# Optimization experiments

Measured on AMD Instinct MI355X. Metric: run time of the kernel, lower is better.

## Reference

```python
import jax, jax.numpy as jnp
import numpy as np

EPS = 1e-5
NUM_HEADS = 8
GN_GROUPS = 32


def _hardswish(x):
    return x * jnp.clip(x + 3.0, 0.0, 6.0) / 6.0


def setup_inputs() -> dict:
    key = jax.random.key(0)
    ks = jax.random.split(key, 12)
    B, C, H, W = 2, 256, 56, 56
    mid, inner = 32, 64  # mid_ca=max(C//8,32); inner=max(C//8, 8*8)//8*8
    s = 0.02
    return {
        "x": jax.random.normal(ks[0], (B, C, H, W), jnp.float32),
        "gate_conv_w": jax.random.normal(ks[1], (mid, C), jnp.float32) * s,
        "bn_gamma": jnp.ones((mid,), jnp.float32),
        "bn_beta": jnp.zeros((mid,), jnp.float32),
        "bn_mean": jax.random.normal(ks[2], (mid,), jnp.float32) * 0.1,
        "bn_var": jax.random.uniform(ks[3], (mid,), jnp.float32) + 0.5,
        "gate_h_w": jax.random.normal(ks[4], (C, mid), jnp.float32) * s,
        "gate_w_w": jax.random.normal(ks[5], (C, mid), jnp.float32) * s,
        "proj_in_w": jax.random.normal(ks[6], (inner, C), jnp.float32) * s,
        "ln_gamma": jnp.ones((inner,), jnp.float32),
        "ln_beta": jnp.zeros((inner,), jnp.float32),
        "wq": jax.random.normal(ks[7], (inner, inner), jnp.float32) * s,
        "wk": jax.random.normal(ks[8], (inner, inner), jnp.float32) * s,
        "wv": jax.random.normal(ks[9], (inner, inner), jnp.float32) * s,
        "proj_out_w": jax.random.normal(ks[10], (C, inner), jnp.float32) * s,
        "gn_gamma": jnp.ones((C,), jnp.float32),
        "gn_beta": jnp.zeros((C,), jnp.float32),
    }


def reference(x, gate_conv_w, bn_gamma, bn_beta, bn_mean, bn_var,
              gate_h_w, gate_w_w, proj_in_w, ln_gamma, ln_beta,
              wq, wk, wv, proj_out_w, gn_gamma, gn_beta):
    B, C, H, W = x.shape
    N = H * W
    inner = proj_in_w.shape[0]
    dh = inner // NUM_HEADS
    scale = dh ** (-0.5)

    # ---- CA gate: pool along W and H, shared 1x1 conv + BN(eval) + hardswish ----
    h_pool = x.mean(axis=3)                      # (B,C,H)
    w_pool = x.mean(axis=2)                      # (B,C,W)
    cat = jnp.concatenate([h_pool, w_pool], axis=2)          # (B,C,H+W)
    cat = jnp.einsum('mc,bcl->bml', gate_conv_w, cat)        # 1x1 conv
    cat = (cat - bn_mean[:, None]) * jax.lax.rsqrt(bn_var[:, None] + EPS)
    cat = cat * bn_gamma[:, None] + bn_beta[:, None]
    cat = _hardswish(cat)
    g_h, g_w = cat[:, :, :H], cat[:, :, H:]                  # (B,mid,H), (B,mid,W)
    gate_h = jax.nn.sigmoid(jnp.einsum('cm,bmh->bch', gate_h_w, g_h))  # (B,C,H)
    gate_w = jax.nn.sigmoid(jnp.einsum('cm,bmw->bcw', gate_w_w, g_w))  # (B,C,W)
    gate = gate_h[:, :, :, None] * gate_w[:, :, None, :]     # (B,C,H,W)

    # ---- projection + layernorm over channel dim ----
    seq = jnp.einsum('ic,bchw->bhwi', proj_in_w, x).reshape(B, N, inner)
    mu = seq.mean(-1, keepdims=True)
    var = seq.var(-1, keepdims=True)  # biased, as torch LayerNorm
    seq = (seq - mu) * jax.lax.rsqrt(var + EPS) * ln_gamma + ln_beta

    gate_spatial = gate.mean(axis=1).reshape(B, N)           # (B,N)

    def heads(w):
        return (seq @ w.T).reshape(B, N, NUM_HEADS, dh).transpose(0, 2, 1, 3)
    q, k, v = heads(wq), heads(wk), heads(wv)                # (B,h,N,dh)

    scores = jnp.einsum('bhnd,bhmd->bhnm', q, k) * scale     # (B,h,N,N)
    gate_bias = jnp.maximum(jnp.log(gate_spatial), -5.0)[:, None, None, :]
    attn = jax.nn.softmax(scores + gate_bias, axis=-1)
    out = jnp.einsum('bhnm,bhmd->bhnd', attn, v)             # (B,h,N,dh)
    out = out.transpose(0, 2, 1, 3).reshape(B, N, inner)
    out = out.transpose(0, 2, 1).reshape(B, inner, H, W)
    out = jnp.einsum('ci,bihw->bchw', proj_out_w, out)       # proj_out 1x1 conv

    # ---- GroupNorm(32, C) ----
    og = out.reshape(B, GN_GROUPS, C // GN_GROUPS, H, W)
    gmu = og.mean((2, 3, 4), keepdims=True)
    gvar = og.var((2, 3, 4), keepdims=True)
    og = (og - gmu) * jax.lax.rsqrt(gvar + EPS)
    out = og.reshape(B, C, H, W) * gn_gamma[None, :, None, None] + gn_beta[None, :, None, None]

    return x + out
```

## Files before the change

kernel.cpp:

```cpp
#include <hip/hip_runtime.h>
#include <math.h>

#define EPSF 1e-5f

constexpr int B_ = 2, C_ = 256, H_ = 56, W_ = 56, N_ = 3136;
constexpr int MID_ = 32, L_ = 112, IN_ = 64, NH_ = 8;

typedef __attribute__((ext_vector_type(8))) __bf16 bf16x8;
typedef __attribute__((ext_vector_type(16))) float f32x16;

constexpr size_t O_POOL = 0;
constexpr size_t O_GH   = O_POOL + (size_t)B_*C_*L_;
constexpr size_t O_GW   = O_GH   + (size_t)B_*C_*H_;
constexpr size_t O_QT   = O_GW   + (size_t)B_*C_*W_;
constexpr size_t O_KT   = O_QT   + (size_t)B_*NH_*N_*16/2;
constexpr size_t O_VT   = O_KT   + (size_t)B_*NH_*N_*16/2;
constexpr size_t O_VZ   = O_VT   + (size_t)B_*NH_*16*N_/2;
constexpr size_t O_OUTC = O_VZ   + N_/2;
constexpr size_t O_GST  = O_OUTC + (size_t)B_*C_*N_/2;
constexpr size_t O_PART = O_GST  + (size_t)B_*32*2;

__device__ inline unsigned pkbf(float lo, float hi) {
  __bf16 a = (__bf16)lo, c = (__bf16)hi;
  return (unsigned)__builtin_bit_cast(unsigned short, a)
       | ((unsigned)__builtin_bit_cast(unsigned short, c) << 16);
}

__device__ inline float bf2f(unsigned short u) {
  unsigned v = (unsigned)u << 16;
  return __builtin_bit_cast(float, v);
}

__device__ inline float fast_exp2(float x) {
#if __has_builtin(__builtin_amdgcn_exp2f)
  return __builtin_amdgcn_exp2f(x);
#else
  float r; asm("v_exp_f32 %0, %1" : "=v"(r) : "v"(x)); return r;
#endif
}

__device__ inline void plane32_swap(unsigned &a, unsigned &b) {
#if __has_builtin(__builtin_amdgcn_permlane32_swap)
  typedef unsigned uv2 __attribute__((ext_vector_type(2)));
  uv2 r = __builtin_amdgcn_permlane32_swap(a, b, false, false);
  a = r.x; b = r.y;
#else
  asm volatile("v_permlane32_swap_b32 %0, %1" : "+v"(a), "+v"(b));
#endif
}

__global__ __launch_bounds__(256) void k_pool(const float* __restrict__ x, float* __restrict__ pool) {
  int bc = blockIdx.x;
  const float4* xp4 = reinterpret_cast<const float4*>(x + (size_t)bc * N_);
  __shared__ float tile[N_];
  float4* t4 = reinterpret_cast<float4*>(tile);
  for (int i = threadIdx.x; i < N_/4; i += 256) t4[i] = xp4[i];
  __syncthreads();
  int t = threadIdx.x;
  if (t < 224) {
    int o = t >> 1, half = t & 1;
    float r = 0.f;
    if (o < 56) {
      const float* row = tile + o*W_ + half*28;
      #pragma unroll 7
      for (int j = 0; j < 28; ++j) r += row[j];
    } else {
      const float* col = tile + (half*28)*W_ + (o - 56);
      #pragma unroll 7
      for (int j = 0; j < 28; ++j) r += col[j*W_];
    }
    r += __shfl_xor(r, 1);
    if (half == 0) pool[(size_t)bc*L_ + o] = r * (1.f/56.f);
  }
}

__global__ __launch_bounds__(256) void k_gates2(const float* __restrict__ gcw, const float* __restrict__ pool,
    const float* __restrict__ bng, const float* __restrict__ bnb,
    const float* __restrict__ bnm, const float* __restrict__ bnv,
    const float* __restrict__ ghw, const float* __restrict__ gww,
    float* __restrict__ ghT, float* __restrict__ gwT) {
  int b = blockIdx.x / H_;
  int p = blockIdx.x % H_;
  __shared__ float cat_s[2][MID_];
  int t = threadIdx.x;
  {
    int out = t >> 2, sub = t & 3;
    int m = out & 31, which = out >> 5;
    int l = p + which*H_;
    const float* pp = pool + (size_t)b*C_*L_ + l;
    const float* wp = gcw + (size_t)m*C_ + sub*64;
    float s = 0.f;
    #pragma unroll 16
    for (int c = 0; c < 64; ++c) s += wp[c] * pp[(size_t)(sub*64 + c)*L_];
    s += __shfl_xor(s, 1); s += __shfl_xor(s, 2);
    if (sub == 0) {
      float xn = (s - bnm[m]) * rsqrtf(bnv[m] + EPSF) * bng[m] + bnb[m];
      cat_s[which][m] = xn * fminf(fmaxf(xn + 3.f, 0.f), 6.f) * (1.f/6.f);
    }
  }
  __syncthreads();
  int c = t;
  float sh = 0.f, sw = 0.f;
  #pragma unroll 8
  for (int m = 0; m < MID_; ++m) {
    sh += ghw[c*MID_ + m] * cat_s[0][m];
    sw += gww[c*MID_ + m] * cat_s[1][m];
  }
  ghT[((size_t)b*H_ + p)*C_ + c] = 1.f/(1.f + expf(-sh));
  gwT[((size_t)b*W_ + p)*C_ + c] = 1.f/(1.f + expf(-sw));
}

__global__ __launch_bounds__(256) void k_fused(const float* __restrict__ x,
    const float* __restrict__ piw, const float* __restrict__ lng, const float* __restrict__ lnb,
    const float* __restrict__ wq, const float* __restrict__ wk, const float* __restrict__ wv,
    const float* __restrict__ ghT, const float* __restrict__ gwT,
    unsigned short* __restrict__ qt, unsigned short* __restrict__ kt,
    unsigned short* __restrict__ vt, unsigned short* __restrict__ vz,
    float* __restrict__ gst) {
  __shared__ __align__(16) unsigned short sT[64][72];
  __shared__ float ps[2][2][64][2];
  __shared__ float lg[64], lb[64];
  __shared__ float bias_s[64];
  int b = blockIdx.x / 49, n0 = (blockIdx.x % 49) * 64;
  int tid = threadIdx.x;
  int wv_ = tid >> 6, lane = tid & 63;
  int m = wv_ & 1, nh = wv_ >> 1, l31 = lane & 31, g = lane >> 5;
  int nloc = nh*32 + l31;
  int nglob = n0 + nloc;
  const float QS = 0.35355339059327373f * 1.4426950408889634f;

  if (tid < 64) { lg[tid] = lng[tid]; lb[tid] = lnb[tid]; }
  if (blockIdx.x == 0 && tid < B_*32*2) gst[tid] = 0.f;

  {
    int px = tid >> 2, sub = tid & 3;
    int n = n0 + px;
    int h = n / W_, w = n % W_;
    const float4* gh4 = reinterpret_cast<const float4*>(ghT + ((size_t)b*H_ + h)*C_ + sub*64);
    const float4* gw4 = reinterpret_cast<const float4*>(gwT + ((size_t)b*W_ + w)*C_ + sub*64);
    float s = 0.f;
    #pragma unroll
    for (int i = 0; i < 16; ++i) {
      float4 a = gh4[i], c2 = gw4[i];
      s += a.x*c2.x + a.y*c2.y + a.z*c2.z + a.w*c2.w;
    }
    s += __shfl_xor(s, 1); s += __shfl_xor(s, 2);
    if (sub == 0)
      bias_s[px] = fmaxf(logf(s * (1.f/C_)), -5.f) * 1.4426950408889634f;
  }
  __syncthreads();

  for (int u = tid; u < 512; u += 256) {
    int h = u >> 6, n = u & 63;
    size_t base = ((size_t)(b*NH_ + h)*N_ + n0 + n)*16;
    *reinterpret_cast<uint4*>(qt + base + 8) = make_uint4(0x3F803F80u, 0u, 0u, 0u);
    float bv = bias_s[n];
    __bf16 bhi = (__bf16)bv; float blo = bv - (float)bhi;
    *reinterpret_cast<uint4*>(kt + base + 8) = make_uint4(pkbf((float)bhi, blo), 0u, 0u, 0u);
  }
  for (int u = tid; u < 512; u += 256) {
    int rr = u >> 3, chunk = u & 7;
    int h = rr >> 3, r = 8 + (rr & 7);
    unsigned val = (r == 8 || r == 12) ? 0x3F803F80u : 0u;
    *reinterpret_cast<uint4*>(vt + ((size_t)(b*NH_+h)*16 + r)*N_ + n0 + chunk*8)
        = make_uint4(val, val, val, val);
  }
  if (b == 0 && tid < 8)
    *reinterpret_cast<uint4*>(vz + n0 + tid*8) = make_uint4(0u, 0u, 0u, 0u);

  const float* arow = piw + (size_t)(32*m + l31)*C_;
  const float* xcol = x + (size_t)b*C_*N_ + nglob;
  f32x16 acc;
  #pragma unroll
  for (int i = 0; i < 16; ++i) acc[i] = 0.f;
  #pragma unroll 4
  for (int kk = 0; kk < 16; ++kk) {
    const float4* ap = reinterpret_cast<const float4*>(arow + kk*16 + g*8);
    float4 a0 = ap[0], a1 = ap[1];
    uint4 au;
    au.x = pkbf(a0.x, a0.y); au.y = pkbf(a0.z, a0.w);
    au.z = pkbf(a1.x, a1.y); au.w = pkbf(a1.z, a1.w);
    float bvl[8];
    #pragma unroll
    for (int e = 0; e < 8; ++e) bvl[e] = xcol[(size_t)(kk*16 + g*8 + e)*N_];
    uint4 bu;
    bu.x = pkbf(bvl[0], bvl[1]); bu.y = pkbf(bvl[2], bvl[3]);
    bu.z = pkbf(bvl[4], bvl[5]); bu.w = pkbf(bvl[6], bvl[7]);
    acc = __builtin_amdgcn_mfma_f32_32x32x16_bf16(
        __builtin_bit_cast(bf16x8, au), __builtin_bit_cast(bf16x8, bu), acc, 0, 0, 0);
  }

  float s = 0.f, ss = 0.f;
  #pragma unroll
  for (int i = 0; i < 16; ++i) { s += acc[i]; ss += acc[i]*acc[i]; }
  ps[m][g][nloc][0] = s; ps[m][g][nloc][1] = ss;
  __syncthreads();
  float S  = ps[0][0][nloc][0] + ps[0][1][nloc][0] + ps[1][0][nloc][0] + ps[1][1][nloc][0];
  float SS = ps[0][0][nloc][1] + ps[0][1][nloc][1] + ps[1][0][nloc][1] + ps[1][1][nloc][1];
  float mu = S * (1.f/IN_);
  float var = SS * (1.f/IN_) - mu*mu;
  float rsd = rsqrtf(var + EPSF);

  #pragma unroll
  for (int cg = 0; cg < 4; ++cg) {
    int jb = 8*cg + 4*g + 32*m;
    float v0 = (acc[cg*4+0]-mu)*rsd*lg[jb+0] + lb[jb+0];
    float v1 = (acc[cg*4+1]-mu)*rsd*lg[jb+1] + lb[jb+1];
    float v2 = (acc[cg*4+2]-mu)*rsd*lg[jb+2] + lb[jb+2];
    float v3 = (acc[cg*4+3]-mu)*rsd*lg[jb+3] + lb[jb+3];
    uint2 w; w.x = pkbf(v0, v1); w.y = pkbf(v2, v3);
    *reinterpret_cast<uint2*>(&sT[nloc][jb]) = w;
  }
  __syncthreads();

  f32x16 aq, ak, av;
  #pragma unroll
  for (int i = 0; i < 16; ++i) { aq[i] = 0.f; ak[i] = 0.f; av[i] = 0.f; }
  const float* qrw = wq + (size_t)(32*m + l31)*IN_;
  const float* krw = wk + (size_t)(32*m + l31)*IN_;
  const float* vrw = wv + (size_t)(32*m + l31)*IN_;
  #pragma unroll
  for (int kk = 0; kk < 4; ++kk) {
    bf16x8 bfr = __builtin_bit_cast(bf16x8,
        *reinterpret_cast<const uint4*>(&sT[nloc][kk*16 + g*8]));
    auto ldA = [&](const float* wrow) {
      const float4* fp = reinterpret_cast<const float4*>(wrow + kk*16 + g*8);
      float4 f0 = fp[0], f1 = fp[1];
      uint4 u;
      u.x = pkbf(f0.x, f0.y); u.y = pkbf(f0.z, f0.w);
      u.z = pkbf(f1.x, f1.y); u.w = pkbf(f1.z, f1.w);
      return __builtin_bit_cast(bf16x8, u);
    };
    aq = __builtin_amdgcn_mfma_f32_32x32x16_bf16(ldA(qrw), bfr, aq, 0, 0, 0);
    ak = __builtin_amdgcn_mfma_f32_32x32x16_bf16(ldA(krw), bfr, ak, 0, 0, 0);
    av = __builtin_amdgcn_mfma_f32_32x32x16_bf16(ldA(vrw), bfr, av, 0, 0, 0);
  }

  #pragma unroll
  for (int cg = 0; cg < 4; ++cg) {
    int h = 4*m + cg, d0 = 4*g;
    size_t rb = ((size_t)(b*NH_ + h)*N_ + nglob)*16 + d0;
    uint2 wqv;
    wqv.x = pkbf(aq[cg*4+0]*QS, aq[cg*4+1]*QS);
    wqv.y = pkbf(aq[cg*4+2]*QS, aq[cg*4+3]*QS);
    *reinterpret_cast<uint2*>(qt + rb) = wqv;
    uint2 wkv;
    wkv.x = pkbf(ak[cg*4+0], ak[cg*4+1]);
    wkv.y = pkbf(ak[cg*4+2], ak[cg*4+3]);
    *reinterpret_cast<uint2*>(kt + rb) = wkv;
    unsigned r0 = pkbf(av[cg*4+0], av[cg*4+1]);
    unsigned r1 = pkbf(av[cg*4+2], av[cg*4+3]);
    size_t vb0 = ((size_t)(b*NH_+h)*16 + d0)*N_ + nglob;
    vt[vb0]                = (unsigned short)r0;
    vt[vb0 + N_]           = (unsigned short)(r0 >> 16);
    vt[vb0 + 2*(size_t)N_] = (unsigned short)r1;
    vt[vb0 + 3*(size_t)N_] = (unsigned short)(r1 >> 16);
  }
}

__global__ __launch_bounds__(256, 4) void k_attn7(const unsigned short* __restrict__ qt,
    const unsigned short* __restrict__ kt, const unsigned short* __restrict__ vt,
    const unsigned short* __restrict__ vz, float* __restrict__ part_g) {
  int tid = threadIdx.x;
  int lane = tid & 63, kh = tid >> 6;
  int l31 = lane & 31, g = lane >> 5;
  int bh = blockIdx.x & 15;
  int rest = blockIdx.x >> 4;
  int qti = rest >> 1, half = rest & 1;
  int qbase = qti * 64;

  bf16x8 qfA = __builtin_bit_cast(bf16x8,
      *reinterpret_cast<const uint4*>(qt + ((size_t)bh*N_ + qbase + l31)*16 + g*8));
  bf16x8 qfB = __builtin_bit_cast(bf16x8,
      *reinterpret_cast<const uint4*>(qt + ((size_t)bh*N_ + qbase + 32 + l31)*16 + g*8));
  f32x16 zf, accA, accB;
  #pragma unroll
  for (int i = 0; i < 16; ++i) { zf[i] = 0.f; accA[i] = 0.f; accB[i] = 0.f; }
  const unsigned short* krow = kt + (size_t)bh*N_*16 + g*8;
  const unsigned short* vbase = (l31 < 16) ? (vt + ((size_t)bh*16 + l31)*(size_t)N_) : vz;

  auto ld = [&](const unsigned short* p) {
    return __builtin_bit_cast(bf16x8, *reinterpret_cast<const uint4*>(p));
  };
  auto halfstep = [&](const f32x16& sa, f32x16& acc, bf16x8 v1, bf16x8 v2) {
    float p[16];
    #pragma unroll
    for (int r = 0; r < 16; ++r) p[r] = fast_exp2(sa[r]);
    unsigned u01 = pkbf(p[0],p[1]),  u23 = pkbf(p[2],p[3]);
    unsigned u45 = pkbf(p[4],p[5]),  u67 = pkbf(p[6],p[7]);
    unsigned u89 = pkbf(p[8],p[9]),  uab = pkbf(p[10],p[11]);
    unsigned ucd = pkbf(p[12],p[13]), uef = pkbf(p[14],p[15]);
    plane32_swap(u01, u45);
    plane32_swap(u23, u67);
    plane32_swap(u89, ucd);
    plane32_swap(uab, uef);
    bf16x8 pf1 = __builtin_bit_cast(bf16x8, make_uint4(u01, u23, u45, u67));
    bf16x8 pf2 = __builtin_bit_cast(bf16x8, make_uint4(u89, uab, ucd, uef));
    acc = __builtin_amdgcn_mfma_f32_32x32x16_bf16(v1, pf1, acc, 0, 0, 0);
    acc = __builtin_amdgcn_mfma_f32_32x32x16_bf16(v2, pf2, acc, 0, 0, 0);
  };

  int tb0 = (half*49 + kh*12) * 32;
  const unsigned short* kp  = krow  + (size_t)(tb0 + l31)*16;
  const unsigned short* vp1 = vbase + tb0 + g*8;
  const unsigned short* vp2 = vp1 + 16;

  bf16x8 kfN = ld(kp), v1N = ld(vp1), v2N = ld(vp2);
  #pragma unroll 4
  for (int j = 0; j < 12; ++j) {
    bf16x8 kf = kfN, v1 = v1N, v2 = v2N;
    if (j < 11) {
      kfN = ld(kp  + (size_t)(j+1)*512);
      v1N = ld(vp1 + (j+1)*32);
      v2N = ld(vp2 + (j+1)*32);
    }
    f32x16 sA = __builtin_amdgcn_mfma_f32_32x32x16_bf16(kf, qfA, zf, 0, 0, 0);
    f32x16 sB = __builtin_amdgcn_mfma_f32_32x32x16_bf16(kf, qfB, zf, 0, 0, 0);
    halfstep(sA, accA, v1, v2);
    halfstep(sB, accB, v1, v2);
  }
  if (kh == 0) {
    int tb = (half*49 + 48) * 32;
    bf16x8 kf = ld(krow + (size_t)(tb + l31)*16);
    bf16x8 v1 = ld(vbase + tb + g*8);
    bf16x8 v2 = ld(vbase + tb + 16 + g*8);
    f32x16 sA = __builtin_amdgcn_mfma_f32_32x32x16_bf16(kf, qfA, zf, 0, 0, 0);
    f32x16 sB = __builtin_amdgcn_mfma_f32_32x32x16_bf16(kf, qfB, zf, 0, 0, 0);
    halfstep(sA, accA, v1, v2);
    halfstep(sB, accB, v1, v2);
  }

  __shared__ float part[3][2][64][5];
  if (kh > 0) {
    #pragma unroll
    for (int j = 0; j < 5; ++j) {
      part[kh-1][0][lane][j] = accA[j];
      part[kh-1][1][lane][j] = accB[j];
    }
  }
  __syncthreads();
  if (kh == 0) {
    float rA[5], rB[5];
    #pragma unroll
    for (int j = 0; j < 5; ++j) { rA[j] = accA[j]; rB[j] = accB[j]; }
    #pragma unroll
    for (int c = 0; c < 3; ++c) {
      #pragma unroll
      for (int j = 0; j < 5; ++j) {
        rA[j] += part[c][0][lane][j];
        rB[j] += part[c][1][lane][j];
      }
    }
    float* pg = part_g + ((((size_t)half*16 + bh)*2 + g)*5)*N_ + qbase + l31;
    #pragma unroll
    for (int j = 0; j < 5; ++j) {
      pg[(size_t)j*N_]      = rA[j];
      pg[(size_t)j*N_ + 32] = rB[j];
    }
  }
}

__global__ __launch_bounds__(128) void k_proj3(const float* __restrict__ part_g,
    const float* __restrict__ pw, unsigned short* __restrict__ outc, float* __restrict__ gst) {
  int bid = blockIdx.x;
  int nb = bid % 49, ct = (bid / 49) % 8, b = bid / (49*8);
  int wave = threadIdx.x >> 6, lane = threadIdx.x & 63;
  int l31 = lane & 31, g = lane >> 5;
  int n0 = nb*64, c0 = ct*32;
  int nw = n0 + wave*32;

  __shared__ float invs[8][64];
  for (int u = threadIdx.x; u < 512; u += 128) {
    int h = u >> 6, n = u & 63;
    size_t r0 = ((((size_t)0*16 + b*8 + h)*2 + 0)*5 + 4)*N_ + n0 + n;
    size_t r1 = ((((size_t)1*16 + b*8 + h)*2 + 0)*5 + 4)*N_ + n0 + n;
    invs[h][n] = 1.f / (part_g[r0] + part_g[r1]);
  }
  __syncthreads();

  const float* wrow = pw + (size_t)(c0 + l31)*IN_;
  bf16x8 afr[4];
  #pragma unroll
  for (int kk = 0; kk < 4; ++kk) {
    const float4* fp = reinterpret_cast<const float4*>(wrow + kk*16 + g*8);
    float4 f0 = fp[0], f1 = fp[1];
    uint4 u;
    u.x = pkbf(f0.x, f0.y); u.y = pkbf(f0.z, f0.w);
    u.z = pkbf(f1.x, f1.y); u.w = pkbf(f1.z, f1.w);
    afr[kk] = __builtin_bit_cast(bf16x8, u);
  }

  f32x16 acc;
  #pragma unroll
  for (int i = 0; i < 16; ++i) acc[i] = 0.f;
  #pragma unroll
  for (int kk = 0; kk < 4; ++kk) {
    int h = kk*2 + g;
    float iv = invs[h][wave*32 + l31];
    const float* p0 = part_g + (((size_t)0*16 + b*8 + h)*2)*5*N_ + nw + l31;
    const float* p1 = part_g + (((size_t)1*16 + b*8 + h)*2)*5*N_ + nw + l31;
    unsigned words[4];
    #pragma unroll
    for (int ep = 0; ep < 4; ++ep) {
      float vv[2];
      #pragma unroll
      for (int e2 = 0; e2 < 2; ++e2) {
        int d = ep*2 + e2;
        int gr = d >> 2, j = d & 3;
        size_t off = ((size_t)gr*5 + j)*N_;
        vv[e2] = (p0[off] + p1[off]) * iv;
      }
      words[ep] = pkbf(vv[0], vv[1]);
    }
    uint4 bu = make_uint4(words[0], words[1], words[2], words[3]);
    acc = __builtin_amdgcn_mfma_f32_32x32x16_bf16(afr[kk], __builtin_bit_cast(bf16x8, bu), acc, 0, 0, 0);
  }

  unsigned short* op = outc + ((size_t)b*C_ + c0)*N_ + nw + l31;
  #pragma unroll
  for (int reg = 0; reg < 16; ++reg) {
    int row = (reg & 3) + 8*(reg >> 2) + 4*g;
    __bf16 vb = (__bf16)acc[reg];
    op[(size_t)row*N_] = __builtin_bit_cast(unsigned short, vb);
  }

  float s4[4], q4[4];
  #pragma unroll
  for (int gl = 0; gl < 4; ++gl) {
    s4[gl] = acc[gl*4+0] + acc[gl*4+1] + acc[gl*4+2] + acc[gl*4+3];
    q4[gl] = acc[gl*4+0]*acc[gl*4+0] + acc[gl*4+1]*acc[gl*4+1]
           + acc[gl*4+2]*acc[gl*4+2] + acc[gl*4+3]*acc[gl*4+3];
  }
  #pragma unroll
  for (int gl = 0; gl < 4; ++gl) {
    #pragma unroll
    for (int off = 32; off > 0; off >>= 1) {
      s4[gl] += __shfl_xor(s4[gl], off);
      q4[gl] += __shfl_xor(q4[gl], off);
    }
  }
  __shared__ float red[2][4][2];
  if (lane == 0) {
    #pragma unroll
    for (int gl = 0; gl < 4; ++gl) { red[wave][gl][0] = s4[gl]; red[wave][gl][1] = q4[gl]; }
  }
  __syncthreads();
  if (threadIdx.x < 8) {
    int gl = threadIdx.x >> 1, which = threadIdx.x & 1;
    float v = red[0][gl][which] + red[1][gl][which];
    atomicAdd(&gst[((size_t)b*32 + ct*4 + gl)*2 + which], v);
  }
}

__global__ __launch_bounds__(256) void k_final(const float* __restrict__ x,
    const unsigned short* __restrict__ outc, const float* __restrict__ gst,
    const float* __restrict__ gng, const float* __restrict__ gnb, float* __restrict__ out) {
  int tid = blockIdx.x*256 + threadIdx.x;
  size_t idx = (size_t)tid * 4;
  int c = (int)((idx / N_) % C_);
  int b = (int)(idx / ((size_t)C_*N_));
  int g = c >> 3;
  float S  = gst[(b*32+g)*2];
  float SS = gst[(b*32+g)*2+1];
  const float invn = 1.f/(8.f*N_);
  float mu = S * invn;
  float var = SS * invn - mu*mu;
  float rs = rsqrtf(var + EPSF);
  float ga = gng[c], be = gnb[c];
  float4 xv = *reinterpret_cast<const float4*>(x + idx);
  uint2 ou = *reinterpret_cast<const uint2*>(outc + idx);
  float o0 = bf2f((unsigned short)(ou.x & 0xffff));
  float o1 = bf2f((unsigned short)(ou.x >> 16));
  float o2 = bf2f((unsigned short)(ou.y & 0xffff));
  float o3 = bf2f((unsigned short)(ou.y >> 16));
  float4 r;
  r.x = xv.x + (o0 - mu)*rs*ga + be;
  r.y = xv.y + (o1 - mu)*rs*ga + be;
  r.z = xv.z + (o2 - mu)*rs*ga + be;
  r.w = xv.w + (o3 - mu)*rs*ga + be;
  *reinterpret_cast<float4*>(out + idx) = r;
}

extern "C" void kernel_launch(void* const* d_in, const int* in_sizes, int n_in,
                              void* d_out, int out_size, void* d_ws, size_t ws_size,
                              hipStream_t stream) {
  const float* x   = (const float*)d_in[0];
  const float* gcw = (const float*)d_in[1];
  const float* bng = (const float*)d_in[2];
  const float* bnb = (const float*)d_in[3];
  const float* bnm = (const float*)d_in[4];
  const float* bnv = (const float*)d_in[5];
  const float* ghw = (const float*)d_in[6];
  const float* gww = (const float*)d_in[7];
  const float* piw = (const float*)d_in[8];
  const float* lng = (const float*)d_in[9];
  const float* lnb = (const float*)d_in[10];
  const float* wq  = (const float*)d_in[11];
  const float* wk  = (const float*)d_in[12];
  const float* wv  = (const float*)d_in[13];
  const float* pw  = (const float*)d_in[14];
  const float* gng = (const float*)d_in[15];
  const float* gnb = (const float*)d_in[16];
  float* ws  = (float*)d_ws;
  float* out = (float*)d_out;
  unsigned short* qt   = (unsigned short*)(ws + O_QT);
  unsigned short* kt   = (unsigned short*)(ws + O_KT);
  unsigned short* vt   = (unsigned short*)(ws + O_VT);
  unsigned short* vz   = (unsigned short*)(ws + O_VZ);
  unsigned short* outc = (unsigned short*)(ws + O_OUTC);

  k_pool<<<B_*C_, 256, 0, stream>>>(x, ws + O_POOL);
  k_gates2<<<B_*H_, 256, 0, stream>>>(gcw, ws+O_POOL, bng, bnb, bnm, bnv, ghw, gww, ws+O_GH, ws+O_GW);
  k_fused<<<B_*49, 256, 0, stream>>>(x, piw, lng, lnb, wq, wk, wv, ws+O_GH, ws+O_GW,
                                     qt, kt, vt, vz, ws+O_GST);
  k_attn7<<<16*98, 256, 0, stream>>>(qt, kt, vt, vz, ws+O_PART);
  k_proj3<<<B_*8*49, 128, 0, stream>>>(ws+O_PART, pw, outc, ws+O_GST);
  k_final<<<(B_*C_*N_)/(4*256), 256, 0, stream>>>(x, outc, ws+O_GST, gng, gnb, out);
}
```

Baseline: 80.57 us.

## Split attention key chunks across single-wave blocks with atomic reduction

The attention kernel previously used 4-wave blocks that reduced their key-split partials through shared memory and a barrier. Each wave is now its own 64-thread block (4x more blocks), and the partials are accumulated with global float atomics into a buffer zeroed inside the pooling kernel. The goal is finer scheduling granularity and no intra-block sync, at the cost of atomic traffic, nondeterministic summation order and extra zeroing work. The final elementwise kernel also processes 8 elements per thread instead of 4.

```diff
diff --git a/kernel.cpp b/kernel.cpp
--- a/kernel.cpp
+++ b/kernel.cpp
@@ -19,6 +19,7 @@
 constexpr size_t O_OUTC = O_VZ   + N_/2;
 constexpr size_t O_GST  = O_OUTC + (size_t)B_*C_*N_/2;
 constexpr size_t O_PART = O_GST  + (size_t)B_*32*2;
+constexpr size_t PART_SZ = (size_t)2*16*2*5*N_;
 
 __device__ inline unsigned pkbf(float lo, float hi) {
   __bf16 a = (__bf16)lo, c = (__bf16)hi;
@@ -49,8 +50,15 @@
 #endif
 }
 
-__global__ __launch_bounds__(256) void k_pool(const float* __restrict__ x, float* __restrict__ pool) {
+__global__ __launch_bounds__(256) void k_pool(const float* __restrict__ x, float* __restrict__ pool,
+                                              float* __restrict__ part_g) {
   int bc = blockIdx.x;
+  {
+    uint4* pg4 = reinterpret_cast<uint4*>(part_g);
+    unsigned total = (unsigned)(PART_SZ / 4);
+    for (unsigned i = bc*256u + threadIdx.x; i < total; i += 512u*256u)
+      pg4[i] = make_uint4(0u, 0u, 0u, 0u);
+  }
   const float4* xp4 = reinterpret_cast<const float4*>(x + (size_t)bc * N_);
   __shared__ float tile[N_];
   float4* t4 = reinterpret_cast<float4*>(tile);
@@ -258,15 +266,16 @@
   }
 }
 
-__global__ __launch_bounds__(256, 4) void k_attn7(const unsigned short* __restrict__ qt,
+__global__ __launch_bounds__(64, 4) void k_attn8(const unsigned short* __restrict__ qt,
     const unsigned short* __restrict__ kt, const unsigned short* __restrict__ vt,
     const unsigned short* __restrict__ vz, float* __restrict__ part_g) {
-  int tid = threadIdx.x;
-  int lane = tid & 63, kh = tid >> 6;
+  int lane = threadIdx.x;
   int l31 = lane & 31, g = lane >> 5;
   int bh = blockIdx.x & 15;
   int rest = blockIdx.x >> 4;
-  int qti = rest >> 1, half = rest & 1;
+  int kh = rest & 3;
+  int half = (rest >> 2) & 1;
+  int qti = rest >> 3;
   int qbase = qti * 64;
 
   bf16x8 qfA = __builtin_bit_cast(bf16x8,
@@ -330,33 +339,11 @@
     halfstep(sB, accB, v1, v2);
   }
 
-  __shared__ float part[3][2][64][5];
-  if (kh > 0) {
-    #pragma unroll
-    for (int j = 0; j < 5; ++j) {
-      part[kh-1][0][lane][j] = accA[j];
-      part[kh-1][1][lane][j] = accB[j];
-    }
-  }
-  __syncthreads();
-  if (kh == 0) {
-    float rA[5], rB[5];
-    #pragma unroll
-    for (int j = 0; j < 5; ++j) { rA[j] = accA[j]; rB[j] = accB[j]; }
-    #pragma unroll
-    for (int c = 0; c < 3; ++c) {
-      #pragma unroll
-      for (int j = 0; j < 5; ++j) {
-        rA[j] += part[c][0][lane][j];
-        rB[j] += part[c][1][lane][j];
-      }
-    }
-    float* pg = part_g + ((((size_t)half*16 + bh)*2 + g)*5)*N_ + qbase + l31;
-    #pragma unroll
-    for (int j = 0; j < 5; ++j) {
-      pg[(size_t)j*N_]      = rA[j];
-      pg[(size_t)j*N_ + 32] = rB[j];
-    }
+  float* pg = part_g + ((((size_t)half*16 + bh)*2 + g)*5)*N_ + qbase + l31;
+  #pragma unroll
+  for (int j = 0; j < 5; ++j) {
+    atomicAdd(&pg[(size_t)j*N_],      accA[j]);
+    atomicAdd(&pg[(size_t)j*N_ + 32], accB[j]);
   }
 }
 
@@ -456,7 +443,7 @@
     const unsigned short* __restrict__ outc, const float* __restrict__ gst,
     const float* __restrict__ gng, const float* __restrict__ gnb, float* __restrict__ out) {
   int tid = blockIdx.x*256 + threadIdx.x;
-  size_t idx = (size_t)tid * 4;
+  size_t idx = (size_t)tid * 8;
   int c = (int)((idx / N_) % C_);
   int b = (int)(idx / ((size_t)C_*N_));
   int g = c >> 3;
@@ -467,18 +454,25 @@
   float var = SS * invn - mu*mu;
   float rs = rsqrtf(var + EPSF);
   float ga = gng[c], be = gnb[c];
-  float4 xv = *reinterpret_cast<const float4*>(x + idx);
-  uint2 ou = *reinterpret_cast<const uint2*>(outc + idx);
-  float o0 = bf2f((unsigned short)(ou.x & 0xffff));
-  float o1 = bf2f((unsigned short)(ou.x >> 16));
-  float o2 = bf2f((unsigned short)(ou.y & 0xffff));
-  float o3 = bf2f((unsigned short)(ou.y >> 16));
-  float4 r;
-  r.x = xv.x + (o0 - mu)*rs*ga + be;
-  r.y = xv.y + (o1 - mu)*rs*ga + be;
-  r.z = xv.z + (o2 - mu)*rs*ga + be;
-  r.w = xv.w + (o3 - mu)*rs*ga + be;
-  *reinterpret_cast<float4*>(out + idx) = r;
+  float4 xv0 = *reinterpret_cast<const float4*>(x + idx);
+  float4 xv1 = *reinterpret_cast<const float4*>(x + idx + 4);
+  uint4 ou = *reinterpret_cast<const uint4*>(outc + idx);
+  float o[8];
+  o[0] = bf2f((unsigned short)(ou.x & 0xffff)); o[1] = bf2f((unsigned short)(ou.x >> 16));
+  o[2] = bf2f((unsigned short)(ou.y & 0xffff)); o[3] = bf2f((unsigned short)(ou.y >> 16));
+  o[4] = bf2f((unsigned short)(ou.z & 0xffff)); o[5] = bf2f((unsigned short)(ou.z >> 16));
+  o[6] = bf2f((unsigned short)(ou.w & 0xffff)); o[7] = bf2f((unsigned short)(ou.w >> 16));
+  float4 r0, r1;
+  r0.x = xv0.x + (o[0] - mu)*rs*ga + be;
+  r0.y = xv0.y + (o[1] - mu)*rs*ga + be;
+  r0.z = xv0.z + (o[2] - mu)*rs*ga + be;
+  r0.w = xv0.w + (o[3] - mu)*rs*ga + be;
+  r1.x = xv1.x + (o[4] - mu)*rs*ga + be;
+  r1.y = xv1.y + (o[5] - mu)*rs*ga + be;
+  r1.z = xv1.z + (o[6] - mu)*rs*ga + be;
+  r1.w = xv1.w + (o[7] - mu)*rs*ga + be;
+  *reinterpret_cast<float4*>(out + idx)     = r0;
+  *reinterpret_cast<float4*>(out + idx + 4) = r1;
 }
 
 extern "C" void kernel_launch(void* const* d_in, const int* in_sizes, int n_in,
@@ -509,11 +503,11 @@
   unsigned short* vz   = (unsigned short*)(ws + O_VZ);
   unsigned short* outc = (unsigned short*)(ws + O_OUTC);
 
-  k_pool<<<B_*C_, 256, 0, stream>>>(x, ws + O_POOL);
+  k_pool<<<B_*C_, 256, 0, stream>>>(x, ws + O_POOL, ws + O_PART);
   k_gates2<<<B_*H_, 256, 0, stream>>>(gcw, ws+O_POOL, bng, bnb, bnm, bnv, ghw, gww, ws+O_GH, ws+O_GW);
   k_fused<<<B_*49, 256, 0, stream>>>(x, piw, lng, lnb, wq, wk, wv, ws+O_GH, ws+O_GW,
                                      qt, kt, vt, vz, ws+O_GST);
-  k_attn7<<<16*98, 256, 0, stream>>>(qt, kt, vt, vz, ws+O_PART);
+  k_attn8<<<16*392, 64, 0, stream>>>(qt, kt, vt, vz, ws+O_PART);
   k_proj3<<<B_*8*49, 128, 0, stream>>>(ws+O_PART, pw, outc, ws+O_GST);
-  k_final<<<(B_*C_*N_)/(4*256), 256, 0, stream>>>(x, outc, ws+O_GST, gng, gnb, out);
-}
+  k_final<<<(B_*C_*N_)/(8*256), 256, 0, stream>>>(x, outc, ws+O_GST, gng, gnb, out);
+}
```

Result: slower. 82.48 us (+2.4%).
